# Performance work log

Hardware: AMD Instinct MI355X
Metric: run time of the kernel (lower is better)

## Reference

```python
import jax, jax.numpy as jnp
import numpy as np

NUM_KNOTS = 64
HEAD_DIM = 4
SCALE = 0.5  # 1/sqrt(4)


def setup_inputs() -> dict:
    key = jax.random.key(0)
    ks = jax.random.split(key, 6)
    B, L, D = 4, 128, 256
    s = 1.0 / np.sqrt(D)
    return {
        "x": jax.random.normal(ks[0], (B, L, D), dtype=jnp.float32),
        "Wq": jax.random.normal(ks[1], (D, D), dtype=jnp.float32) * s,
        "Wk": jax.random.normal(ks[2], (D, D), dtype=jnp.float32) * s,
        "Wv": jax.random.normal(ks[3], (D, D), dtype=jnp.float32) * s,
        "Wo": jax.random.normal(ks[4], (D, D), dtype=jnp.float32) * s,
        "bo": jnp.zeros((D,), dtype=jnp.float32),
    }


def reference(x, Wq, Wk, Wv, Wo, bo):
    # x: [B, L, D], D = NUM_KNOTS * HEAD_DIM = 256
    B, L, D = x.shape
    N = L * NUM_KNOTS  # flattened 'knot' sequence length
    # nn.Linear applies x @ W.T
    q = (x @ Wq.T).reshape(B, N, HEAD_DIM)
    k = (x @ Wk.T).reshape(B, N, HEAD_DIM)
    v = (x @ Wv.T).reshape(B, N, HEAD_DIM)
    # full attention over the length-N knot sequence (head_dim = 4)
    logits = jnp.einsum("bnd,bmd->bnm", q, k) * SCALE  # [B, N, N]
    attn = jax.nn.softmax(logits, axis=-1)
    out = jnp.einsum("bnm,bmd->bnd", attn, v).reshape(B, L, D)
    return out @ Wo.T + bo
```

## Files before the change

kernel.cpp:

```cpp
#include <hip/hip_runtime.h>

#define NQ 8192
#define BLROWS 512
#define DIM 256
#define KSLICES 16

#define QSCALE 0.7213475204444817f

typedef float v2f __attribute__((ext_vector_type(2)));

__device__ __forceinline__ float ex2(float x) {
#if __has_builtin(__builtin_amdgcn_exp2f)
    return __builtin_amdgcn_exp2f(x);
#else
    return exp2f(x);
#endif
}

__global__ __launch_bounds__(256) void qkv_proj(
    const float* __restrict__ x,
    const float* __restrict__ Wq, const float* __restrict__ Wk,
    const float* __restrict__ Wv,
    float* __restrict__ Qb, float* __restrict__ Kb, float* __restrict__ Vb)
{
    const int m = blockIdx.y;
    const float* W = (m == 0) ? Wq : (m == 1) ? Wk : Wv;
    float* C       = (m == 0) ? Qb : (m == 1) ? Kb : Vb;
    const float sc = (m == 0) ? QSCALE : 1.0f;
    const int j  = threadIdx.x;
    const int rb = blockIdx.x * 4;

    float acc[4] = {0.f, 0.f, 0.f, 0.f};
    const float4* __restrict__ W4 = reinterpret_cast<const float4*>(W + j * DIM);
    const float*  __restrict__ A0 = x + rb * DIM;

    #pragma unroll 4
    for (int d4 = 0; d4 < DIM / 4; ++d4) {
        const float4 w = W4[d4];
        #pragma unroll
        for (int r = 0; r < 4; ++r) {
            const float4 a = reinterpret_cast<const float4*>(A0 + r * DIM)[d4];
            acc[r] = fmaf(a.x, w.x, acc[r]);
            acc[r] = fmaf(a.y, w.y, acc[r]);
            acc[r] = fmaf(a.z, w.z, acc[r]);
            acc[r] = fmaf(a.w, w.w, acc[r]);
        }
    }
    #pragma unroll
    for (int r = 0; r < 4; ++r)
        C[(rb + r) * DIM + j] = acc[r] * sc;
}

__global__ __launch_bounds__(256, 6) void attn_partial(
    const float* __restrict__ Q, const float* __restrict__ K,
    const float* __restrict__ V, float* __restrict__ P)
{
    __shared__ float4 KV[1024];
    __shared__ float  red2[4][256];

    const int t    = threadIdx.x;
    const int lane = t & 63;
    const int w    = __builtin_amdgcn_readfirstlane(t >> 6);
    const int qt   = blockIdx.x;
    const int ks   = blockIdx.y;
    const int b    = blockIdx.z;

    {
        const float4* __restrict__ Kg = reinterpret_cast<const float4*>(K) + b * NQ + ks * 512;
        const float4* __restrict__ Vg = reinterpret_cast<const float4*>(V) + b * NQ + ks * 512;
        KV[t]             = Kg[t];
        KV[t + 256]       = Kg[t + 256];
        KV[512 + t]       = Vg[t];
        KV[512 + t + 256] = Vg[t + 256];
    }

    const float4* __restrict__ Qp = reinterpret_cast<const float4*>(Q) + b * NQ + qt * 256;
    v2f qx[2], qy[2], qz[2], qw[2];
    #pragma unroll
    for (int p = 0; p < 2; ++p) {
        const float4 t0 = Qp[(2 * p)     * 64 + lane];
        const float4 t1 = Qp[(2 * p + 1) * 64 + lane];
        qx[p] = v2f{t0.x, t1.x};
        qy[p] = v2f{t0.y, t1.y};
        qz[p] = v2f{t0.z, t1.z};
        qw[p] = v2f{t0.w, t1.w};
    }
    v2f a0[2], a1[2], a2[2], a3[2], ls[2];
    #pragma unroll
    for (int p = 0; p < 2; ++p) {
        a0[p] = v2f{0.f, 0.f}; a1[p] = v2f{0.f, 0.f};
        a2[p] = v2f{0.f, 0.f}; a3[p] = v2f{0.f, 0.f};
        ls[p] = v2f{0.f, 0.f};
    }
    __syncthreads();

    const float4* __restrict__ Kl = &KV[w * 128];
    const float4* __restrict__ Vl = &KV[512 + w * 128];

    #pragma unroll 4
    for (int j = 0; j < 128; ++j) {
        const float4 k4 = Kl[j];
        const float4 v4 = Vl[j];
        #pragma unroll
        for (int p = 0; p < 2; ++p) {
            v2f s = qx[p] * k4.x;
            s = __builtin_elementwise_fma(qy[p], v2f{k4.y, k4.y}, s);
            s = __builtin_elementwise_fma(qz[p], v2f{k4.z, k4.z}, s);
            s = __builtin_elementwise_fma(qw[p], v2f{k4.w, k4.w}, s);
            const v2f e = v2f{ex2(s[0]), ex2(s[1])};
            ls[p] += e;
            a0[p] = __builtin_elementwise_fma(e, v2f{v4.x, v4.x}, a0[p]);
            a1[p] = __builtin_elementwise_fma(e, v2f{v4.y, v4.y}, a1[p]);
            a2[p] = __builtin_elementwise_fma(e, v2f{v4.z, v4.z}, a2[p]);
            a3[p] = __builtin_elementwise_fma(e, v2f{v4.w, v4.w}, a3[p]);
        }
    }

    float* __restrict__ Pb = P + (size_t)((b * KSLICES + ks) * 5) * NQ + qt * 256;
    __syncthreads();

#define RED_ROUND(ARR, cidx)                                              \
    {                                                                     \
        _Pragma("unroll")                                                 \
        for (int p = 0; p < 2; ++p) {                                     \
            _Pragma("unroll")                                             \
            for (int e = 0; e < 2; ++e)                                   \
                red2[w][(2 * p + e) * 64 + lane] = ARR[p][e];             \
        }                                                                 \
        __syncthreads();                                                  \
        Pb[(cidx) * NQ + t] =                                             \
            red2[0][t] + red2[1][t] + red2[2][t] + red2[3][t];            \
        __syncthreads();                                                  \
    }

    RED_ROUND(ls, 0)
    RED_ROUND(a0, 1)
    RED_ROUND(a1, 2)
    RED_ROUND(a2, 3)
    RED_ROUND(a3, 4)
#undef RED_ROUND
}

__global__ __launch_bounds__(256) void merge_oproj(
    const float* __restrict__ P, const float* __restrict__ Wo,
    const float* __restrict__ bo, float* __restrict__ out)
{
    __shared__ float aoL[4][DIM];

    const int rb = blockIdx.x * 4;
    const int b  = rb >> 7;
    const int n0 = (rb & 127) * 64;
    const int t  = threadIdx.x;

    {
        float sums[5] = {0.f, 0.f, 0.f, 0.f, 0.f};
        const float* __restrict__ Pb = P + (size_t)(b * KSLICES * 5) * NQ + n0 + t;
        #pragma unroll
        for (int s = 0; s < KSLICES; ++s) {
            #pragma unroll
            for (int c = 0; c < 5; ++c)
                sums[c] += Pb[(s * 5 + c) * NQ];
        }
        const float inv = 1.0f / sums[0];
        const int row = t >> 6;
        const int d0  = (t & 63) * 4;
        aoL[row][d0 + 0] = sums[1] * inv;
        aoL[row][d0 + 1] = sums[2] * inv;
        aoL[row][d0 + 2] = sums[3] * inv;
        aoL[row][d0 + 3] = sums[4] * inv;
    }
    __syncthreads();

    const int j = t;
    float acc[4] = {0.f, 0.f, 0.f, 0.f};
    const float4* __restrict__ W4 = reinterpret_cast<const float4*>(Wo + j * DIM);
    #pragma unroll 4
    for (int d4 = 0; d4 < DIM / 4; ++d4) {
        const float4 wv = W4[d4];
        #pragma unroll
        for (int r = 0; r < 4; ++r) {
            const float4 a = reinterpret_cast<const float4*>(&aoL[r][0])[d4];
            acc[r] = fmaf(a.x, wv.x, acc[r]);
            acc[r] = fmaf(a.y, wv.y, acc[r]);
            acc[r] = fmaf(a.z, wv.z, acc[r]);
            acc[r] = fmaf(a.w, wv.w, acc[r]);
        }
    }
    const float bias = bo[j];
    #pragma unroll
    for (int r = 0; r < 4; ++r)
        out[(rb + r) * DIM + j] = acc[r] + bias;
}

extern "C" void kernel_launch(void* const* d_in, const int* in_sizes, int n_in,
                              void* d_out, int out_size, void* d_ws, size_t ws_size,
                              hipStream_t stream) {
    const float* x  = (const float*)d_in[0];
    const float* Wq = (const float*)d_in[1];
    const float* Wk = (const float*)d_in[2];
    const float* Wv = (const float*)d_in[3];
    const float* Wo = (const float*)d_in[4];
    const float* bo = (const float*)d_in[5];
    float* out = (float*)d_out;

    float* Qb = (float*)d_ws;
    float* Kb = Qb + BLROWS * DIM;
    float* Vb = Kb + BLROWS * DIM;
    float* P  = Vb + BLROWS * DIM;

    qkv_proj<<<dim3(128, 3), 256, 0, stream>>>(x, Wq, Wk, Wv, Qb, Kb, Vb);
    attn_partial<<<dim3(32, KSLICES, 4), 256, 0, stream>>>(Qb, Kb, Vb, P);
    merge_oproj<<<128, 256, 0, stream>>>(P, Wo, bo, out);
}
```

Measured before the change: 91.56 us.

## Store K/V in SoA shared memory and vectorize over keys instead of queries

K and V tiles are transposed into structure-of-arrays shared buffers so each thread reads four consecutive keys per component with a 128-bit load. The packed FMA dimension now runs across pairs of keys with broadcast query values, and each thread handles four queries. This cuts the per-key broadcast packing and shares each LDS load across more work. It adds more accumulator registers (8 queries' worth split into lo/hi pairs) and lowers the occupancy hint from 6 to 4 waves per SIMD, with a final lo+hi reduction before the shared-memory sum.

```diff
diff --git a/kernel.cpp b/kernel.cpp
--- a/kernel.cpp
+++ b/kernel.cpp
@@ -8,6 +8,7 @@
 #define QSCALE 0.7213475204444817f
 
 typedef float v2f __attribute__((ext_vector_type(2)));
+typedef float v4f __attribute__((ext_vector_type(4)));
 
 __device__ __forceinline__ float ex2(float x) {
 #if __has_builtin(__builtin_amdgcn_exp2f)
@@ -51,12 +52,13 @@
         C[(rb + r) * DIM + j] = acc[r] * sc;
 }
 
-__global__ __launch_bounds__(256, 6) void attn_partial(
+__global__ __launch_bounds__(256, 4) void attn_partial(
     const float* __restrict__ Q, const float* __restrict__ K,
     const float* __restrict__ V, float* __restrict__ P)
 {
-    __shared__ float4 KV[1024];
-    __shared__ float  red2[4][256];
+    __shared__ __align__(16) float Ksoa[4][512];
+    __shared__ __align__(16) float Vsoa[4][512];
+    __shared__ float red2[4][256];
 
     const int t    = threadIdx.x;
     const int lane = t & 63;
@@ -68,51 +70,77 @@
     {
         const float4* __restrict__ Kg = reinterpret_cast<const float4*>(K) + b * NQ + ks * 512;
         const float4* __restrict__ Vg = reinterpret_cast<const float4*>(V) + b * NQ + ks * 512;
-        KV[t]             = Kg[t];
-        KV[t + 256]       = Kg[t + 256];
-        KV[512 + t]       = Vg[t];
-        KV[512 + t + 256] = Vg[t + 256];
+        const float4 k0 = Kg[t], k1 = Kg[t + 256];
+        const float4 v0 = Vg[t], v1 = Vg[t + 256];
+        Ksoa[0][t] = k0.x; Ksoa[1][t] = k0.y; Ksoa[2][t] = k0.z; Ksoa[3][t] = k0.w;
+        Ksoa[0][t + 256] = k1.x; Ksoa[1][t + 256] = k1.y; Ksoa[2][t + 256] = k1.z; Ksoa[3][t + 256] = k1.w;
+        Vsoa[0][t] = v0.x; Vsoa[1][t] = v0.y; Vsoa[2][t] = v0.z; Vsoa[3][t] = v0.w;
+        Vsoa[0][t + 256] = v1.x; Vsoa[1][t + 256] = v1.y; Vsoa[2][t + 256] = v1.z; Vsoa[3][t + 256] = v1.w;
     }
 
     const float4* __restrict__ Qp = reinterpret_cast<const float4*>(Q) + b * NQ + qt * 256;
-    v2f qx[2], qy[2], qz[2], qw[2];
-    #pragma unroll
-    for (int p = 0; p < 2; ++p) {
-        const float4 t0 = Qp[(2 * p)     * 64 + lane];
-        const float4 t1 = Qp[(2 * p + 1) * 64 + lane];
-        qx[p] = v2f{t0.x, t1.x};
-        qy[p] = v2f{t0.y, t1.y};
-        qz[p] = v2f{t0.z, t1.z};
-        qw[p] = v2f{t0.w, t1.w};
-    }
-    v2f a0[2], a1[2], a2[2], a3[2], ls[2];
-    #pragma unroll
-    for (int p = 0; p < 2; ++p) {
-        a0[p] = v2f{0.f, 0.f}; a1[p] = v2f{0.f, 0.f};
-        a2[p] = v2f{0.f, 0.f}; a3[p] = v2f{0.f, 0.f};
-        ls[p] = v2f{0.f, 0.f};
+    v2f qx2[4], qy2[4], qz2[4], qw2[4];
+    #pragma unroll
+    for (int r = 0; r < 4; ++r) {
+        const float4 q = Qp[r * 64 + lane];
+        qx2[r] = v2f{q.x, q.x};
+        qy2[r] = v2f{q.y, q.y};
+        qz2[r] = v2f{q.z, q.z};
+        qw2[r] = v2f{q.w, q.w};
+    }
+    v2f ls2[4], a02[4], a12[4], a22[4], a32[4];
+    #pragma unroll
+    for (int r = 0; r < 4; ++r) {
+        ls2[r] = v2f{0.f, 0.f};
+        a02[r] = v2f{0.f, 0.f}; a12[r] = v2f{0.f, 0.f};
+        a22[r] = v2f{0.f, 0.f}; a32[r] = v2f{0.f, 0.f};
     }
     __syncthreads();
 
-    const float4* __restrict__ Kl = &KV[w * 128];
-    const float4* __restrict__ Vl = &KV[512 + w * 128];
-
-    #pragma unroll 4
-    for (int j = 0; j < 128; ++j) {
-        const float4 k4 = Kl[j];
-        const float4 v4 = Vl[j];
-        #pragma unroll
-        for (int p = 0; p < 2; ++p) {
-            v2f s = qx[p] * k4.x;
-            s = __builtin_elementwise_fma(qy[p], v2f{k4.y, k4.y}, s);
-            s = __builtin_elementwise_fma(qz[p], v2f{k4.z, k4.z}, s);
-            s = __builtin_elementwise_fma(qw[p], v2f{k4.w, k4.w}, s);
-            const v2f e = v2f{ex2(s[0]), ex2(s[1])};
-            ls[p] += e;
-            a0[p] = __builtin_elementwise_fma(e, v2f{v4.x, v4.x}, a0[p]);
-            a1[p] = __builtin_elementwise_fma(e, v2f{v4.y, v4.y}, a1[p]);
-            a2[p] = __builtin_elementwise_fma(e, v2f{v4.z, v4.z}, a2[p]);
-            a3[p] = __builtin_elementwise_fma(e, v2f{v4.w, v4.w}, a3[p]);
+    const int kbase = w * 128;
+
+    #pragma unroll 2
+    for (int jj = 0; jj < 32; ++jj) {
+        const int j = kbase + jj * 4;
+        const v4f kx4 = *reinterpret_cast<const v4f*>(&Ksoa[0][j]);
+        const v4f ky4 = *reinterpret_cast<const v4f*>(&Ksoa[1][j]);
+        const v4f kz4 = *reinterpret_cast<const v4f*>(&Ksoa[2][j]);
+        const v4f kw4 = *reinterpret_cast<const v4f*>(&Ksoa[3][j]);
+        const v4f vx4 = *reinterpret_cast<const v4f*>(&Vsoa[0][j]);
+        const v4f vy4 = *reinterpret_cast<const v4f*>(&Vsoa[1][j]);
+        const v4f vz4 = *reinterpret_cast<const v4f*>(&Vsoa[2][j]);
+        const v4f vw4 = *reinterpret_cast<const v4f*>(&Vsoa[3][j]);
+        const v2f kxlo = __builtin_shufflevector(kx4, kx4, 0, 1), kxhi = __builtin_shufflevector(kx4, kx4, 2, 3);
+        const v2f kylo = __builtin_shufflevector(ky4, ky4, 0, 1), kyhi = __builtin_shufflevector(ky4, ky4, 2, 3);
+        const v2f kzlo = __builtin_shufflevector(kz4, kz4, 0, 1), kzhi = __builtin_shufflevector(kz4, kz4, 2, 3);
+        const v2f kwlo = __builtin_shufflevector(kw4, kw4, 0, 1), kwhi = __builtin_shufflevector(kw4, kw4, 2, 3);
+        const v2f vxlo = __builtin_shufflevector(vx4, vx4, 0, 1), vxhi = __builtin_shufflevector(vx4, vx4, 2, 3);
+        const v2f vylo = __builtin_shufflevector(vy4, vy4, 0, 1), vyhi = __builtin_shufflevector(vy4, vy4, 2, 3);
+        const v2f vzlo = __builtin_shufflevector(vz4, vz4, 0, 1), vzhi = __builtin_shufflevector(vz4, vz4, 2, 3);
+        const v2f vwlo = __builtin_shufflevector(vw4, vw4, 0, 1), vwhi = __builtin_shufflevector(vw4, vw4, 2, 3);
+
+        #pragma unroll
+        for (int r = 0; r < 4; ++r) {
+            v2f slo = kxlo * qx2[r];
+            slo = __builtin_elementwise_fma(kylo, qy2[r], slo);
+            slo = __builtin_elementwise_fma(kzlo, qz2[r], slo);
+            slo = __builtin_elementwise_fma(kwlo, qw2[r], slo);
+            v2f shi = kxhi * qx2[r];
+            shi = __builtin_elementwise_fma(kyhi, qy2[r], shi);
+            shi = __builtin_elementwise_fma(kzhi, qz2[r], shi);
+            shi = __builtin_elementwise_fma(kwhi, qw2[r], shi);
+            const v2f e01 = v2f{ex2(slo[0]), ex2(slo[1])};
+            const v2f e23 = v2f{ex2(shi[0]), ex2(shi[1])};
+            ls2[r] += e01;
+            ls2[r] += e23;
+            a02[r] = __builtin_elementwise_fma(e01, vxlo, a02[r]);
+            a02[r] = __builtin_elementwise_fma(e23, vxhi, a02[r]);
+            a12[r] = __builtin_elementwise_fma(e01, vylo, a12[r]);
+            a12[r] = __builtin_elementwise_fma(e23, vyhi, a12[r]);
+            a22[r] = __builtin_elementwise_fma(e01, vzlo, a22[r]);
+            a22[r] = __builtin_elementwise_fma(e23, vzhi, a22[r]);
+            a32[r] = __builtin_elementwise_fma(e01, vwlo, a32[r]);
+            a32[r] = __builtin_elementwise_fma(e23, vwhi, a32[r]);
         }
     }
 
@@ -122,22 +150,19 @@
 #define RED_ROUND(ARR, cidx)                                              \
     {                                                                     \
         _Pragma("unroll")                                                 \
-        for (int p = 0; p < 2; ++p) {                                     \
-            _Pragma("unroll")                                             \
-            for (int e = 0; e < 2; ++e)                                   \
-                red2[w][(2 * p + e) * 64 + lane] = ARR[p][e];             \
-        }                                                                 \
+        for (int r = 0; r < 4; ++r)                                       \
+            red2[w][r * 64 + lane] = ARR[r][0] + ARR[r][1];               \
         __syncthreads();                                                  \
         Pb[(cidx) * NQ + t] =                                             \
             red2[0][t] + red2[1][t] + red2[2][t] + red2[3][t];            \
         __syncthreads();                                                  \
     }
 
-    RED_ROUND(ls, 0)
-    RED_ROUND(a0, 1)
-    RED_ROUND(a1, 2)
-    RED_ROUND(a2, 3)
-    RED_ROUND(a3, 4)
+    RED_ROUND(ls2, 0)
+    RED_ROUND(a02, 1)
+    RED_ROUND(a12, 2)
+    RED_ROUND(a22, 3)
+    RED_ROUND(a32, 4)
 #undef RED_ROUND
 }
 
```

Measured after the change: 91.59 us. Within noise of the previous version (+0.0%).
